# Optimization experiments

Measured on AMD Instinct MI355X. Metric: run time of the kernel, lower is better.

The kernel has to match this reference:

```python
import jax, jax.numpy as jnp
import numpy as np

N, B, H, NH = 16384, 64, 256, 8
MAXN = 512
EPS = 1e-5


def setup_inputs() -> dict:
    key = jax.random.key(0)
    ks = jax.random.split(key, 8)
    s = 0.02
    return {
        "x": jax.random.normal(ks[0], (N, H), jnp.float32),
        "batch": jnp.sort(jax.random.randint(ks[1], (N,), 0, B)),
        "max_nodes": MAXN,
        "norm1_w": jnp.ones((H,), jnp.float32),
        "norm1_b": jnp.zeros((H,), jnp.float32),
        "in_proj_w": jax.random.normal(ks[2], (3 * H, H), jnp.float32) * s,
        "in_proj_b": jnp.zeros((3 * H,), jnp.float32),
        "out_proj_w": jax.random.normal(ks[3], (H, H), jnp.float32) * s,
        "out_proj_b": jnp.zeros((H,), jnp.float32),
        "norm2_w": jnp.ones((H,), jnp.float32),
        "norm2_b": jnp.zeros((H,), jnp.float32),
        "ffn_w1": jax.random.normal(ks[4], (4 * H, H), jnp.float32) * s,
        "ffn_b1": jnp.zeros((4 * H,), jnp.float32),
        "ffn_w2": jax.random.normal(ks[5], (H, 4 * H), jnp.float32) * s,
        "ffn_b2": jnp.zeros((H,), jnp.float32),
    }


def _graph_norm(x, batch, countsf, w, b):
    # Per-graph mean and unbiased std (torch.std default), eps added to std.
    mean = jax.ops.segment_sum(x, batch, num_segments=B) / countsf[:, None]
    c = x - mean[batch]
    var = jax.ops.segment_sum(c * c, batch, num_segments=B) / jnp.maximum(countsf - 1.0, 1.0)[:, None]
    std = jnp.sqrt(var) + EPS
    return w * (c / std[batch]) + b


def _forward(x, batch, max_nodes, norm1_w, norm1_b, in_proj_w, in_proj_b,
             out_proj_w, out_proj_b, norm2_w, norm2_b, ffn_w1, ffn_b1, ffn_w2, ffn_b2):
    n = x.shape[0]
    counts = jax.ops.segment_sum(jnp.ones((n,), jnp.int32), batch, num_segments=B)  # [B]
    countsf = counts.astype(x.dtype)
    starts = jnp.concatenate([jnp.zeros((1,), jnp.int32), jnp.cumsum(counts)[:-1]])
    pos = jnp.arange(n, dtype=jnp.int32) - starts[batch]  # position within graph (batch is sorted)

    # GraphNorm 1, then pack ragged -> padded [B, M, H]
    xn = _graph_norm(x, batch, countsf, norm1_w, norm1_b)
    x_pad = jnp.zeros((B, max_nodes, H), x.dtype).at[batch, pos].set(xn)
    key_valid = jnp.arange(max_nodes)[None, :] < counts[:, None]  # [B, M] True=real node

    # Multi-head attention (eval mode, key_padding_mask)
    qkv = x_pad @ in_proj_w.T + in_proj_b  # [B, M, 3H]
    q, k, v = jnp.split(qkv, 3, axis=-1)
    hd = H // NH
    heads = lambda t: t.reshape(B, max_nodes, NH, hd).transpose(0, 2, 1, 3)  # [B, NH, M, hd]
    q, k, v = heads(q), heads(k), heads(v)
    scores = jnp.einsum('bhqd,bhkd->bhqk', q, k) / np.float32(np.sqrt(hd))
    scores = jnp.where(key_valid[:, None, None, :], scores, jnp.float32(-1e9))
    attn = jax.nn.softmax(scores, axis=-1)
    ctx = jnp.einsum('bhqk,bhkd->bhqd', attn, v).transpose(0, 2, 1, 3).reshape(B, max_nodes, H)
    attn_out = ctx @ out_proj_w.T + out_proj_b

    # Unpack padded -> ragged, residual
    x = x + attn_out[batch, pos]

    # GraphNorm 2 + FFN (exact GELU) + residual
    xn2 = _graph_norm(x, batch, countsf, norm2_w, norm2_b)
    h = jax.nn.gelu(xn2 @ ffn_w1.T + ffn_b1, approximate=False)
    return x + (h @ ffn_w2.T + ffn_b2)


def reference(x, batch, max_nodes, norm1_w, norm1_b, in_proj_w, in_proj_b,
              out_proj_w, out_proj_b, norm2_w, norm2_b, ffn_w1, ffn_b1, ffn_w2, ffn_b2):
    return _forward(x, batch, max_nodes, norm1_w, norm1_b, in_proj_w, in_proj_b,
                    out_proj_w, out_proj_b, norm2_w, norm2_b, ffn_w1, ffn_b1, ffn_w2, ffn_b2)
```

## Files before the change

kernel.cpp:

```cpp
#include <hip/hip_runtime.h>
#include <hip/hip_bf16.h>
#include <math.h>

typedef __bf16 bf16;
typedef bf16 bf16x4 __attribute__((ext_vector_type(4)));
typedef bf16 bf16x8 __attribute__((ext_vector_type(8)));
typedef float f32x4 __attribute__((ext_vector_type(4)));

#define NNODES 16384
#define NB 64
#define HDIM 256
#define NHEADS 8
#define HD 32
#define GN_STRIPS 16

typedef __attribute__((address_space(3))) unsigned int lds_u32;
typedef __attribute__((address_space(1))) const unsigned int glb_u32;

__device__ __forceinline__ void async_copy16(const bf16* gsrc, bf16* ldst) {
    __builtin_amdgcn_global_load_lds((glb_u32*)gsrc, (lds_u32*)ldst, 16, 0, 0);
}

__global__ void cvt_all(const float* __restrict__ pw_q, const float* __restrict__ pw_o,
                        const float* __restrict__ pw_1, const float* __restrict__ pw_2,
                        bf16* __restrict__ dq, bf16* __restrict__ d_o,
                        bf16* __restrict__ d1, bf16* __restrict__ d2,
                        const int* __restrict__ batch, int* __restrict__ starts,
                        int* __restrict__ counts) {
    if (blockIdx.x == 0 && threadIdx.x < 64) {
        int b = threadIdx.x;
        int lo = 0, hi = NNODES;
        while (lo < hi) { int mid = (lo + hi) >> 1; if (batch[mid] < b) lo = mid + 1; else hi = mid; }
        int s0 = lo;
        lo = 0; hi = NNODES;
        while (lo < hi) { int mid = (lo + hi) >> 1; if (batch[mid] < b + 1) lo = mid + 1; else hi = mid; }
        starts[b] = s0;
        counts[b] = lo - s0;
    }
    int i = blockIdx.x * 256 + threadIdx.x;
    const float* src; bf16* dst; int j;
    if (i < 49152)       { src = pw_q; dst = dq;  j = i; }
    else if (i < 65536)  { src = pw_o; dst = d_o; j = i - 49152; }
    else if (i < 131072) { src = pw_1; dst = d1;  j = i - 65536; }
    else                 { src = pw_2; dst = d2;  j = i - 131072; }
    float4 v = *(const float4*)(src + (size_t)j * 4);
    bf16x4 o;
    o[0] = (bf16)v.x; o[1] = (bf16)v.y; o[2] = (bf16)v.z; o[3] = (bf16)v.w;
    *(bf16x4*)(dst + (size_t)j * 4) = o;
}

__global__ __launch_bounds__(256) void gn_partial(
    const float* __restrict__ x, const int* __restrict__ starts,
    const int* __restrict__ counts, float* __restrict__ part) {
    int g = blockIdx.x, strip = blockIdx.y, hh = threadIdx.x;
    int s = starts[g], c = counts[g];
    int chunk = (c + GN_STRIPS - 1) / GN_STRIPS;
    int r0 = strip * chunk, r1 = min(c, r0 + chunk);
    float sum = 0.f, sq = 0.f;
    for (int r = r0; r < r1; ++r) {
        float v = x[(size_t)(s + r) * HDIM + hh];
        sum += v; sq += v * v;
    }
    part[((size_t)(g * GN_STRIPS + strip) * 2 + 0) * HDIM + hh] = sum;
    part[((size_t)(g * GN_STRIPS + strip) * 2 + 1) * HDIM + hh] = sq;
}

__global__ __launch_bounds__(256) void gn_final(
    const float* __restrict__ part, const int* __restrict__ counts,
    const float* __restrict__ w, const float* __restrict__ b, float* __restrict__ stats) {
    int g = blockIdx.x, hh = threadIdx.x;
    float sum = 0.f, sq = 0.f;
    for (int st = 0; st < GN_STRIPS; ++st) {
        sum += part[((size_t)(g * GN_STRIPS + st) * 2 + 0) * HDIM + hh];
        sq  += part[((size_t)(g * GN_STRIPS + st) * 2 + 1) * HDIM + hh];
    }
    float cf = (float)counts[g];
    float mean = sum / cf;
    float var = (sq - cf * mean * mean) / fmaxf(cf - 1.f, 1.f);
    var = fmaxf(var, 0.f);
    float inv = 1.f / (sqrtf(var) + 1e-5f);
    float a = w[hh] * inv;
    stats[(size_t)g * 512 + hh] = a;
    stats[(size_t)g * 512 + 256 + hh] = b[hh] - mean * a;
}

__global__ __launch_bounds__(256) void gn_apply(
    const float* __restrict__ x, const int* __restrict__ batch,
    const float* __restrict__ stats, bf16* __restrict__ out) {
    size_t i = ((size_t)blockIdx.x * 256 + threadIdx.x) * 4;
    int row = (int)(i >> 8);
    int g = batch[row];
    int hh = (int)(i & 255);
    float4 xv = *(const float4*)(x + i);
    float4 av = *(const float4*)(stats + (size_t)g * 512 + hh);
    float4 bv = *(const float4*)(stats + (size_t)g * 512 + 256 + hh);
    bf16x4 o;
    o[0] = (bf16)(av.x * xv.x + bv.x);
    o[1] = (bf16)(av.y * xv.y + bv.y);
    o[2] = (bf16)(av.z * xv.z + bv.z);
    o[3] = (bf16)(av.w * xv.w + bv.w);
    *(bf16x4*)(out + i) = o;
}

template <int MODE>
__global__ __launch_bounds__(256) void gemm_tn(
    const bf16* __restrict__ A, const bf16* __restrict__ B,
    const float* __restrict__ bias, const float* __restrict__ res,
    void* __restrict__ Cout, int M, int N, int K) {
    __shared__ __align__(16) bf16 As[128 * 32];
    __shared__ __align__(16) bf16 Bs[128 * 32];
    const int row0 = blockIdx.x * 128;
    const int col0 = blockIdx.y * 128;
    const int tid = threadIdx.x;
    const int lane = tid & 63;
    const int wave = tid >> 6;
    const int wm = (wave >> 1) * 64;
    const int wn = (wave & 1) * 64;
    const int lr = lane & 15;
    const int lk = lane >> 4;
    const int c0 = tid;
    const int c1 = tid + 256;
    const int r0c = c0 >> 2, o0 = (c0 & 3) * 8;
    const int r1c = c1 >> 2, o1 = (c1 & 3) * 8;

    const bf16* Ab = A + (size_t)row0 * K;
    const bf16* Bb = B + (size_t)col0 * K;

    f32x4 acc[4][4] = {};

    for (int k0 = 0; k0 < K; k0 += 32) {
        __syncthreads();
        async_copy16(Ab + (size_t)r0c * K + k0 + o0, &As[c0 * 8]);
        async_copy16(Ab + (size_t)r1c * K + k0 + o1, &As[c1 * 8]);
        async_copy16(Bb + (size_t)r0c * K + k0 + o0, &Bs[c0 * 8]);
        async_copy16(Bb + (size_t)r1c * K + k0 + o1, &Bs[c1 * 8]);
        __syncthreads();
        bf16x8 af[4], bfr[4];
#pragma unroll
        for (int mi = 0; mi < 4; ++mi)
            af[mi] = *(const bf16x8*)&As[(wm + mi * 16 + lr) * 32 + lk * 8];
#pragma unroll
        for (int ni = 0; ni < 4; ++ni)
            bfr[ni] = *(const bf16x8*)&Bs[(wn + ni * 16 + lr) * 32 + lk * 8];
#pragma unroll
        for (int mi = 0; mi < 4; ++mi)
#pragma unroll
            for (int ni = 0; ni < 4; ++ni)
                acc[mi][ni] = __builtin_amdgcn_mfma_f32_16x16x32_bf16(af[mi], bfr[ni], acc[mi][ni], 0, 0, 0);
    }

#pragma unroll
    for (int mi = 0; mi < 4; ++mi) {
#pragma unroll
        for (int ni = 0; ni < 4; ++ni) {
            const int col = col0 + wn + ni * 16 + lr;
            const float bv = bias[col];
#pragma unroll
            for (int r = 0; r < 4; ++r) {
                const int row = row0 + wm + mi * 16 + lk * 4 + r;
                float v = acc[mi][ni][r] + bv;
                size_t idx = (size_t)row * N + col;
                if (MODE == 0) {
                    ((bf16*)Cout)[idx] = (bf16)v;
                } else if (MODE == 1) {
                    ((float*)Cout)[idx] = v + res[idx];
                } else {
                    float gel = 0.5f * v * (1.f + erff(v * 0.70710678118654752f));
                    ((bf16*)Cout)[idx] = (bf16)gel;
                }
            }
        }
    }
}

__global__ __launch_bounds__(256) void gemm_small_res(
    const bf16* __restrict__ A, const bf16* __restrict__ B,
    const float* __restrict__ bias, const float* __restrict__ res,
    float* __restrict__ Cout, int M, int N, int K) {
    __shared__ __align__(16) bf16 As[64 * 32];
    __shared__ __align__(16) bf16 Bs[64 * 32];
    const int row0 = blockIdx.x * 64;
    const int col0 = blockIdx.y * 64;
    const int tid = threadIdx.x;
    const int lane = tid & 63;
    const int wave = tid >> 6;
    const int wr = (wave >> 1) * 32;
    const int wc = (wave & 1) * 32;
    const int lr = lane & 15;
    const int lk = lane >> 4;
    const int rs = tid >> 2, os = (tid & 3) * 8;

    const bf16* Ab = A + (size_t)row0 * K;
    const bf16* Bb = B + (size_t)col0 * K;

    f32x4 acc[2][2] = {};

    for (int k0 = 0; k0 < K; k0 += 32) {
        __syncthreads();
        async_copy16(Ab + (size_t)rs * K + k0 + os, &As[tid * 8]);
        async_copy16(Bb + (size_t)rs * K + k0 + os, &Bs[tid * 8]);
        __syncthreads();
        bf16x8 af[2], bfr[2];
#pragma unroll
        for (int mi = 0; mi < 2; ++mi)
            af[mi] = *(const bf16x8*)&As[(wr + mi * 16 + lr) * 32 + lk * 8];
#pragma unroll
        for (int ni = 0; ni < 2; ++ni)
            bfr[ni] = *(const bf16x8*)&Bs[(wc + ni * 16 + lr) * 32 + lk * 8];
#pragma unroll
        for (int mi = 0; mi < 2; ++mi)
#pragma unroll
            for (int ni = 0; ni < 2; ++ni)
                acc[mi][ni] = __builtin_amdgcn_mfma_f32_16x16x32_bf16(af[mi], bfr[ni], acc[mi][ni], 0, 0, 0);
    }

#pragma unroll
    for (int mi = 0; mi < 2; ++mi) {
#pragma unroll
        for (int ni = 0; ni < 2; ++ni) {
            const int col = col0 + wc + ni * 16 + lr;
            const float bv = bias[col];
#pragma unroll
            for (int r = 0; r < 4; ++r) {
                const int row = row0 + wr + mi * 16 + lk * 4 + r;
                size_t idx = (size_t)row * N + col;
                Cout[idx] = acc[mi][ni][r] + bv + res[idx];
            }
        }
    }
}

__global__ __launch_bounds__(256) void attn_mfma(
    const bf16* __restrict__ qkv, const int* __restrict__ starts,
    const int* __restrict__ counts, bf16* __restrict__ ctx) {
    int g = blockIdx.x, h = blockIdx.y;
    int s = starts[g], c = counts[g];
    if (c <= 0) return;
    __shared__ __align__(16) bf16 Qs[256][40];
    __shared__ __align__(16) bf16 Ks[64][40];
    __shared__ __align__(16) bf16 Vt[32][72];
    __shared__ __align__(16) bf16 Ps[4][64][72];
    __shared__ float Ls[4][64];
    const int tid = threadIdx.x;
    const int w = tid >> 6, lane = tid & 63;
    const int lo = lane & 15, hi = lane >> 4;
    const float scale = 0.17677669529663687f;
    const int nqc = (c + 255) >> 8;
    const int nkt = (c + 63) >> 6;

    for (int qc = 0; qc < nqc; ++qc) {
        {
            int qrow = qc * 256 + tid;
            const bf16* qp = qkv + (size_t)(s + qrow) * 768 + h * HD;
#pragma unroll
            for (int t4 = 0; t4 < 4; ++t4) {
                bf16x8 sv;
                if (qrow < c) {
                    bf16x8 v = *(const bf16x8*)(qp + t4 * 8);
#pragma unroll
                    for (int u = 0; u < 8; ++u) sv[u] = (bf16)((float)v[u] * scale);
                } else {
#pragma unroll
                    for (int u = 0; u < 8; ++u) sv[u] = (bf16)0.f;
                }
                *(bf16x8*)&Qs[tid][t4 * 8] = sv;
            }
        }
        __syncthreads();
        bf16x8 bq[4];
#pragma unroll
        for (int nt = 0; nt < 4; ++nt) bq[nt] = *(const bf16x8*)&Qs[w * 64 + nt * 16 + lo][hi * 8];

        f32x4 ctxa[4][2] = {};
        float l[4] = {0.f, 0.f, 0.f, 0.f};

        for (int kt = 0; kt < nkt; ++kt) {
            {
                int krow = kt * 64 + (tid >> 2);
                bf16x8 v;
                if (krow < c) v = *(const bf16x8*)(qkv + (size_t)(s + krow) * 768 + 256 + h * HD + (tid & 3) * 8);
                else {
#pragma unroll
                    for (int u = 0; u < 8; ++u) v[u] = (bf16)0.f;
                }
                *(bf16x8*)&Ks[tid >> 2][(tid & 3) * 8] = v;
            }
            {
                int vrow = kt * 64 + (tid & 63);
                int dg = tid >> 6;
                bf16x8 v;
                if (vrow < c) v = *(const bf16x8*)(qkv + (size_t)(s + vrow) * 768 + 512 + h * HD + dg * 8);
                else {
#pragma unroll
                    for (int u = 0; u < 8; ++u) v[u] = (bf16)0.f;
                }
#pragma unroll
                for (int u = 0; u < 8; ++u) Vt[dg * 8 + u][tid & 63] = v[u];
            }
            __syncthreads();

            f32x4 sacc[4][4] = {};
#pragma unroll
            for (int kmt = 0; kmt < 4; ++kmt) {
                bf16x8 ak = *(const bf16x8*)&Ks[kmt * 16 + lo][hi * 8];
#pragma unroll
                for (int nt = 0; nt < 4; ++nt)
                    sacc[kmt][nt] = __builtin_amdgcn_mfma_f32_16x16x32_bf16(ak, bq[nt], sacc[kmt][nt], 0, 0, 0);
            }
#pragma unroll
            for (int kmt = 0; kmt < 4; ++kmt) {
                int kbase = kt * 64 + kmt * 16 + hi * 4;
#pragma unroll
                for (int nt = 0; nt < 4; ++nt) {
                    bf16x4 pv;
#pragma unroll
                    for (int r = 0; r < 4; ++r) {
                        float p = (kbase + r < c) ? __expf(sacc[kmt][nt][r]) : 0.f;
                        l[nt] += p;
                        pv[r] = (bf16)p;
                    }
                    *(bf16x4*)&Ps[w][nt * 16 + lo][kmt * 16 + hi * 4] = pv;
                }
            }
#pragma unroll
            for (int ks = 0; ks < 2; ++ks) {
                bf16x8 bv[2];
#pragma unroll
                for (int dn = 0; dn < 2; ++dn) bv[dn] = *(const bf16x8*)&Vt[dn * 16 + lo][ks * 32 + hi * 8];
#pragma unroll
                for (int qmt = 0; qmt < 4; ++qmt) {
                    bf16x8 ap = *(const bf16x8*)&Ps[w][qmt * 16 + lo][ks * 32 + hi * 8];
#pragma unroll
                    for (int dn = 0; dn < 2; ++dn)
                        ctxa[qmt][dn] = __builtin_amdgcn_mfma_f32_16x16x32_bf16(ap, bv[dn], ctxa[qmt][dn], 0, 0, 0);
                }
            }
            __syncthreads();
        }

#pragma unroll
        for (int nt = 0; nt < 4; ++nt) {
            l[nt] += __shfl_xor(l[nt], 16);
            l[nt] += __shfl_xor(l[nt], 32);
        }
        if (hi == 0) {
#pragma unroll
            for (int nt = 0; nt < 4; ++nt) Ls[w][nt * 16 + lo] = l[nt];
        }
#pragma unroll
        for (int qmt = 0; qmt < 4; ++qmt) {
#pragma unroll
            for (int r = 0; r < 4; ++r) {
                int qrow = qc * 256 + w * 64 + qmt * 16 + hi * 4 + r;
                if (qrow < c) {
                    float linv = 1.f / Ls[w][qmt * 16 + hi * 4 + r];
                    bf16* op = ctx + (size_t)(s + qrow) * HDIM + h * HD;
#pragma unroll
                    for (int dn = 0; dn < 2; ++dn)
                        op[dn * 16 + lo] = (bf16)(ctxa[qmt][dn][r] * linv);
                }
            }
        }
        __syncthreads();
    }
}

extern "C" void kernel_launch(void* const* d_in, const int* in_sizes, int n_in,
                              void* d_out, int out_size, void* d_ws, size_t ws_size,
                              hipStream_t stream) {
    const float* x        = (const float*)d_in[0];
    const int*   batch    = (const int*)d_in[1];
    const float* norm1_w  = (const float*)d_in[3];
    const float* norm1_b  = (const float*)d_in[4];
    const float* in_proj_w  = (const float*)d_in[5];
    const float* in_proj_b  = (const float*)d_in[6];
    const float* out_proj_w = (const float*)d_in[7];
    const float* out_proj_b = (const float*)d_in[8];
    const float* norm2_w  = (const float*)d_in[9];
    const float* norm2_b  = (const float*)d_in[10];
    const float* ffn_w1   = (const float*)d_in[11];
    const float* ffn_b1   = (const float*)d_in[12];
    const float* ffn_w2   = (const float*)d_in[13];
    const float* ffn_b2   = (const float*)d_in[14];
    float* out = (float*)d_out;

    char* ws = (char*)d_ws;
    size_t off = 0;
    auto alloc = [&](size_t bytes) -> void* {
        void* p = ws + off;
        off += bytes;
        off = (off + 255) & ~(size_t)255;
        return p;
    };
    int*  starts = (int*)alloc(NB * 4);
    int*  counts = (int*)alloc(NB * 4);
    bf16* wq = (bf16*)alloc((size_t)768 * 256 * 2);
    bf16* wo = (bf16*)alloc((size_t)256 * 256 * 2);
    bf16* w1 = (bf16*)alloc((size_t)1024 * 256 * 2);
    bf16* w2 = (bf16*)alloc((size_t)256 * 1024 * 2);
    bf16* t0  = (bf16*)alloc((size_t)NNODES * HDIM * 2);
    bf16* qkv = (bf16*)alloc((size_t)NNODES * 768 * 2);
    float* y  = (float*)alloc((size_t)NNODES * HDIM * 4);
    bf16* hbuf = (bf16*)alloc((size_t)NNODES * 1024 * 2);
    float* gnpart = (float*)alloc((size_t)NB * GN_STRIPS * 2 * HDIM * 4);
    float* gnstats = (float*)alloc((size_t)NB * 512 * 4);

    cvt_all<<<196608 / 256, 256, 0, stream>>>(in_proj_w, out_proj_w, ffn_w1, ffn_w2,
                                              wq, wo, w1, w2, batch, starts, counts);
    gn_partial<<<dim3(NB, GN_STRIPS), 256, 0, stream>>>(x, starts, counts, gnpart);
    gn_final<<<NB, 256, 0, stream>>>(gnpart, counts, norm1_w, norm1_b, gnstats);
    gn_apply<<<NNODES * HDIM / 1024, 256, 0, stream>>>(x, batch, gnstats, t0);
    gemm_tn<0><<<dim3(NNODES / 128, 768 / 128), 256, 0, stream>>>(
        t0, wq, in_proj_b, nullptr, qkv, NNODES, 768, 256);
    attn_mfma<<<dim3(NB, NHEADS), 256, 0, stream>>>(qkv, starts, counts, t0);
    gemm_small_res<<<dim3(NNODES / 64, 256 / 64), 256, 0, stream>>>(
        t0, wo, out_proj_b, x, y, NNODES, 256, 256);
    gn_partial<<<dim3(NB, GN_STRIPS), 256, 0, stream>>>(y, starts, counts, gnpart);
    gn_final<<<NB, 256, 0, stream>>>(gnpart, counts, norm2_w, norm2_b, gnstats);
    gn_apply<<<NNODES * HDIM / 1024, 256, 0, stream>>>(y, batch, gnstats, t0);
    gemm_tn<2><<<dim3(NNODES / 128, 1024 / 128), 256, 0, stream>>>(
        t0, w1, ffn_b1, nullptr, hbuf, NNODES, 1024, 256);
    gemm_small_res<<<dim3(NNODES / 64, 256 / 64), 256, 0, stream>>>(
        hbuf, w2, ffn_b2, y, out, NNODES, 256, 1024);
}
```

Before: 237.2 us.

## Double GEMM K-tile with XOR-swizzled LDS and split attention query chunks across blocks

Both GEMM kernels now stage 64-wide K tiles instead of 32, which halves the number of barrier pairs per output tile. They store the tiles in LDS with an XOR swizzle on 16-byte chunks to avoid bank conflicts on the fragment reads. The attention kernel moves its query-chunk loop onto a third grid dimension of size 2, so graphs with more than 256 nodes run on separate blocks and there are more blocks in flight. The cost is double the LDS per GEMM block, which may reduce occupancy, and extra blocks that exit immediately for small graphs.

```diff
diff --git a/kernel.cpp b/kernel.cpp
--- a/kernel.cpp
+++ b/kernel.cpp
@@ -107,8 +107,8 @@
     const bf16* __restrict__ A, const bf16* __restrict__ B,
     const float* __restrict__ bias, const float* __restrict__ res,
     void* __restrict__ Cout, int M, int N, int K) {
-    __shared__ __align__(16) bf16 As[128 * 32];
-    __shared__ __align__(16) bf16 Bs[128 * 32];
+    __shared__ __align__(16) bf16 As[128 * 64];
+    __shared__ __align__(16) bf16 Bs[128 * 64];
     const int row0 = blockIdx.x * 128;
     const int col0 = blockIdx.y * 128;
     const int tid = threadIdx.x;
@@ -118,35 +118,49 @@
     const int wn = (wave & 1) * 64;
     const int lr = lane & 15;
     const int lk = lane >> 4;
-    const int c0 = tid;
-    const int c1 = tid + 256;
-    const int r0c = c0 >> 2, o0 = (c0 & 3) * 8;
-    const int r1c = c1 >> 2, o1 = (c1 & 3) * 8;
 
     const bf16* Ab = A + (size_t)row0 * K;
     const bf16* Bb = B + (size_t)col0 * K;
 
+    int srow[4], soff[4];
+#pragma unroll
+    for (int q = 0; q < 4; ++q) {
+        int c = tid + q * 256;
+        int r = c >> 3;
+        srow[q] = r;
+        soff[q] = ((c & 7) ^ (r & 7)) * 8;
+    }
+
     f32x4 acc[4][4] = {};
 
-    for (int k0 = 0; k0 < K; k0 += 32) {
-        __syncthreads();
-        async_copy16(Ab + (size_t)r0c * K + k0 + o0, &As[c0 * 8]);
-        async_copy16(Ab + (size_t)r1c * K + k0 + o1, &As[c1 * 8]);
-        async_copy16(Bb + (size_t)r0c * K + k0 + o0, &Bs[c0 * 8]);
-        async_copy16(Bb + (size_t)r1c * K + k0 + o1, &Bs[c1 * 8]);
-        __syncthreads();
-        bf16x8 af[4], bfr[4];
-#pragma unroll
-        for (int mi = 0; mi < 4; ++mi)
-            af[mi] = *(const bf16x8*)&As[(wm + mi * 16 + lr) * 32 + lk * 8];
-#pragma unroll
-        for (int ni = 0; ni < 4; ++ni)
-            bfr[ni] = *(const bf16x8*)&Bs[(wn + ni * 16 + lr) * 32 + lk * 8];
-#pragma unroll
-        for (int mi = 0; mi < 4; ++mi)
-#pragma unroll
-            for (int ni = 0; ni < 4; ++ni)
-                acc[mi][ni] = __builtin_amdgcn_mfma_f32_16x16x32_bf16(af[mi], bfr[ni], acc[mi][ni], 0, 0, 0);
+    for (int k0 = 0; k0 < K; k0 += 64) {
+        __syncthreads();
+#pragma unroll
+        for (int q = 0; q < 4; ++q)
+            async_copy16(Ab + (size_t)srow[q] * K + k0 + soff[q], &As[(tid + q * 256) * 8]);
+#pragma unroll
+        for (int q = 0; q < 4; ++q)
+            async_copy16(Bb + (size_t)srow[q] * K + k0 + soff[q], &Bs[(tid + q * 256) * 8]);
+        __syncthreads();
+#pragma unroll
+        for (int ks = 0; ks < 2; ++ks) {
+            bf16x8 af[4], bfr[4];
+#pragma unroll
+            for (int mi = 0; mi < 4; ++mi) {
+                int r = wm + mi * 16 + lr;
+                af[mi] = *(const bf16x8*)&As[r * 64 + ((ks * 4 + lk) ^ (r & 7)) * 8];
+            }
+#pragma unroll
+            for (int ni = 0; ni < 4; ++ni) {
+                int r = wn + ni * 16 + lr;
+                bfr[ni] = *(const bf16x8*)&Bs[r * 64 + ((ks * 4 + lk) ^ (r & 7)) * 8];
+            }
+#pragma unroll
+            for (int mi = 0; mi < 4; ++mi)
+#pragma unroll
+                for (int ni = 0; ni < 4; ++ni)
+                    acc[mi][ni] = __builtin_amdgcn_mfma_f32_16x16x32_bf16(af[mi], bfr[ni], acc[mi][ni], 0, 0, 0);
+        }
     }
 
 #pragma unroll
@@ -177,8 +191,8 @@
     const bf16* __restrict__ A, const bf16* __restrict__ B,
     const float* __restrict__ bias, const float* __restrict__ res,
     float* __restrict__ Cout, int M, int N, int K) {
-    __shared__ __align__(16) bf16 As[64 * 32];
-    __shared__ __align__(16) bf16 Bs[64 * 32];
+    __shared__ __align__(16) bf16 As[64 * 64];
+    __shared__ __align__(16) bf16 Bs[64 * 64];
     const int row0 = blockIdx.x * 64;
     const int col0 = blockIdx.y * 64;
     const int tid = threadIdx.x;
@@ -188,30 +202,49 @@
     const int wc = (wave & 1) * 32;
     const int lr = lane & 15;
     const int lk = lane >> 4;
-    const int rs = tid >> 2, os = (tid & 3) * 8;
 
     const bf16* Ab = A + (size_t)row0 * K;
     const bf16* Bb = B + (size_t)col0 * K;
 
+    int srow[2], soff[2];
+#pragma unroll
+    for (int q = 0; q < 2; ++q) {
+        int c = tid + q * 256;
+        int r = c >> 3;
+        srow[q] = r;
+        soff[q] = ((c & 7) ^ (r & 7)) * 8;
+    }
+
     f32x4 acc[2][2] = {};
 
-    for (int k0 = 0; k0 < K; k0 += 32) {
-        __syncthreads();
-        async_copy16(Ab + (size_t)rs * K + k0 + os, &As[tid * 8]);
-        async_copy16(Bb + (size_t)rs * K + k0 + os, &Bs[tid * 8]);
-        __syncthreads();
-        bf16x8 af[2], bfr[2];
-#pragma unroll
-        for (int mi = 0; mi < 2; ++mi)
-            af[mi] = *(const bf16x8*)&As[(wr + mi * 16 + lr) * 32 + lk * 8];
-#pragma unroll
-        for (int ni = 0; ni < 2; ++ni)
-            bfr[ni] = *(const bf16x8*)&Bs[(wc + ni * 16 + lr) * 32 + lk * 8];
-#pragma unroll
-        for (int mi = 0; mi < 2; ++mi)
-#pragma unroll
-            for (int ni = 0; ni < 2; ++ni)
-                acc[mi][ni] = __builtin_amdgcn_mfma_f32_16x16x32_bf16(af[mi], bfr[ni], acc[mi][ni], 0, 0, 0);
+    for (int k0 = 0; k0 < K; k0 += 64) {
+        __syncthreads();
+#pragma unroll
+        for (int q = 0; q < 2; ++q)
+            async_copy16(Ab + (size_t)srow[q] * K + k0 + soff[q], &As[(tid + q * 256) * 8]);
+#pragma unroll
+        for (int q = 0; q < 2; ++q)
+            async_copy16(Bb + (size_t)srow[q] * K + k0 + soff[q], &Bs[(tid + q * 256) * 8]);
+        __syncthreads();
+#pragma unroll
+        for (int ks = 0; ks < 2; ++ks) {
+            bf16x8 af[2], bfr[2];
+#pragma unroll
+            for (int mi = 0; mi < 2; ++mi) {
+                int r = wr + mi * 16 + lr;
+                af[mi] = *(const bf16x8*)&As[r * 64 + ((ks * 4 + lk) ^ (r & 7)) * 8];
+            }
+#pragma unroll
+            for (int ni = 0; ni < 2; ++ni) {
+                int r = wc + ni * 16 + lr;
+                bfr[ni] = *(const bf16x8*)&Bs[r * 64 + ((ks * 4 + lk) ^ (r & 7)) * 8];
+            }
+#pragma unroll
+            for (int mi = 0; mi < 2; ++mi)
+#pragma unroll
+                for (int ni = 0; ni < 2; ++ni)
+                    acc[mi][ni] = __builtin_amdgcn_mfma_f32_16x16x32_bf16(af[mi], bfr[ni], acc[mi][ni], 0, 0, 0);
+        }
     }
 
 #pragma unroll
@@ -233,9 +266,9 @@
 __global__ __launch_bounds__(256) void attn_mfma(
     const bf16* __restrict__ qkv, const int* __restrict__ starts,
     const int* __restrict__ counts, bf16* __restrict__ ctx) {
-    int g = blockIdx.x, h = blockIdx.y;
+    int g = blockIdx.x, h = blockIdx.y, qc = blockIdx.z;
     int s = starts[g], c = counts[g];
-    if (c <= 0) return;
+    if (qc * 256 >= c) return;
     __shared__ __align__(16) bf16 Qs[256][40];
     __shared__ __align__(16) bf16 Ks[64][40];
     __shared__ __align__(16) bf16 Vt[32][72];
@@ -245,123 +278,119 @@
     const int w = tid >> 6, lane = tid & 63;
     const int lo = lane & 15, hi = lane >> 4;
     const float scale = 0.17677669529663687f;
-    const int nqc = (c + 255) >> 8;
     const int nkt = (c + 63) >> 6;
 
-    for (int qc = 0; qc < nqc; ++qc) {
+    {
+        int qrow = qc * 256 + tid;
+        const bf16* qp = qkv + (size_t)(s + qrow) * 768 + h * HD;
+#pragma unroll
+        for (int t4 = 0; t4 < 4; ++t4) {
+            bf16x8 sv;
+            if (qrow < c) {
+                bf16x8 v = *(const bf16x8*)(qp + t4 * 8);
+#pragma unroll
+                for (int u = 0; u < 8; ++u) sv[u] = (bf16)((float)v[u] * scale);
+            } else {
+#pragma unroll
+                for (int u = 0; u < 8; ++u) sv[u] = (bf16)0.f;
+            }
+            *(bf16x8*)&Qs[tid][t4 * 8] = sv;
+        }
+    }
+    __syncthreads();
+    bf16x8 bq[4];
+#pragma unroll
+    for (int nt = 0; nt < 4; ++nt) bq[nt] = *(const bf16x8*)&Qs[w * 64 + nt * 16 + lo][hi * 8];
+
+    f32x4 ctxa[4][2] = {};
+    float l[4] = {0.f, 0.f, 0.f, 0.f};
+
+    for (int kt = 0; kt < nkt; ++kt) {
         {
-            int qrow = qc * 256 + tid;
-            const bf16* qp = qkv + (size_t)(s + qrow) * 768 + h * HD;
-#pragma unroll
-            for (int t4 = 0; t4 < 4; ++t4) {
-                bf16x8 sv;
-                if (qrow < c) {
-                    bf16x8 v = *(const bf16x8*)(qp + t4 * 8);
-#pragma unroll
-                    for (int u = 0; u < 8; ++u) sv[u] = (bf16)((float)v[u] * scale);
-                } else {
-#pragma unroll
-                    for (int u = 0; u < 8; ++u) sv[u] = (bf16)0.f;
+            int krow = kt * 64 + (tid >> 2);
+            bf16x8 v;
+            if (krow < c) v = *(const bf16x8*)(qkv + (size_t)(s + krow) * 768 + 256 + h * HD + (tid & 3) * 8);
+            else {
+#pragma unroll
+                for (int u = 0; u < 8; ++u) v[u] = (bf16)0.f;
+            }
+            *(bf16x8*)&Ks[tid >> 2][(tid & 3) * 8] = v;
+        }
+        {
+            int vrow = kt * 64 + (tid & 63);
+            int dg = tid >> 6;
+            bf16x8 v;
+            if (vrow < c) v = *(const bf16x8*)(qkv + (size_t)(s + vrow) * 768 + 512 + h * HD + dg * 8);
+            else {
+#pragma unroll
+                for (int u = 0; u < 8; ++u) v[u] = (bf16)0.f;
+            }
+#pragma unroll
+            for (int u = 0; u < 8; ++u) Vt[dg * 8 + u][tid & 63] = v[u];
+        }
+        __syncthreads();
+
+        f32x4 sacc[4][4] = {};
+#pragma unroll
+        for (int kmt = 0; kmt < 4; ++kmt) {
+            bf16x8 ak = *(const bf16x8*)&Ks[kmt * 16 + lo][hi * 8];
+#pragma unroll
+            for (int nt = 0; nt < 4; ++nt)
+                sacc[kmt][nt] = __builtin_amdgcn_mfma_f32_16x16x32_bf16(ak, bq[nt], sacc[kmt][nt], 0, 0, 0);
+        }
+#pragma unroll
+        for (int kmt = 0; kmt < 4; ++kmt) {
+            int kbase = kt * 64 + kmt * 16 + hi * 4;
+#pragma unroll
+            for (int nt = 0; nt < 4; ++nt) {
+                bf16x4 pv;
+#pragma unroll
+                for (int r = 0; r < 4; ++r) {
+                    float p = (kbase + r < c) ? __expf(sacc[kmt][nt][r]) : 0.f;
+                    l[nt] += p;
+                    pv[r] = (bf16)p;
                 }
-                *(bf16x8*)&Qs[tid][t4 * 8] = sv;
-            }
-        }
-        __syncthreads();
-        bf16x8 bq[4];
-#pragma unroll
-        for (int nt = 0; nt < 4; ++nt) bq[nt] = *(const bf16x8*)&Qs[w * 64 + nt * 16 + lo][hi * 8];
-
-        f32x4 ctxa[4][2] = {};
-        float l[4] = {0.f, 0.f, 0.f, 0.f};
-
-        for (int kt = 0; kt < nkt; ++kt) {
-            {
-                int krow = kt * 64 + (tid >> 2);
-                bf16x8 v;
-                if (krow < c) v = *(const bf16x8*)(qkv + (size_t)(s + krow) * 768 + 256 + h * HD + (tid & 3) * 8);
-                else {
-#pragma unroll
-                    for (int u = 0; u < 8; ++u) v[u] = (bf16)0.f;
-                }
-                *(bf16x8*)&Ks[tid >> 2][(tid & 3) * 8] = v;
-            }
-            {
-                int vrow = kt * 64 + (tid & 63);
-                int dg = tid >> 6;
-                bf16x8 v;
-                if (vrow < c) v = *(const bf16x8*)(qkv + (size_t)(s + vrow) * 768 + 512 + h * HD + dg * 8);
-                else {
-#pragma unroll
-                    for (int u = 0; u < 8; ++u) v[u] = (bf16)0.f;
-                }
-#pragma unroll
-                for (int u = 0; u < 8; ++u) Vt[dg * 8 + u][tid & 63] = v[u];
-            }
-            __syncthreads();
-
-            f32x4 sacc[4][4] = {};
-#pragma unroll
-            for (int kmt = 0; kmt < 4; ++kmt) {
-                bf16x8 ak = *(const bf16x8*)&Ks[kmt * 16 + lo][hi * 8];
-#pragma unroll
-                for (int nt = 0; nt < 4; ++nt)
-                    sacc[kmt][nt] = __builtin_amdgcn_mfma_f32_16x16x32_bf16(ak, bq[nt], sacc[kmt][nt], 0, 0, 0);
-            }
-#pragma unroll
-            for (int kmt = 0; kmt < 4; ++kmt) {
-                int kbase = kt * 64 + kmt * 16 + hi * 4;
-#pragma unroll
-                for (int nt = 0; nt < 4; ++nt) {
-                    bf16x4 pv;
-#pragma unroll
-                    for (int r = 0; r < 4; ++r) {
-                        float p = (kbase + r < c) ? __expf(sacc[kmt][nt][r]) : 0.f;
-                        l[nt] += p;
-                        pv[r] = (bf16)p;
-                    }
-                    *(bf16x4*)&Ps[w][nt * 16 + lo][kmt * 16 + hi * 4] = pv;
-                }
-            }
-#pragma unroll
-            for (int ks = 0; ks < 2; ++ks) {
-                bf16x8 bv[2];
-#pragma unroll
-                for (int dn = 0; dn < 2; ++dn) bv[dn] = *(const bf16x8*)&Vt[dn * 16 + lo][ks * 32 + hi * 8];
-#pragma unroll
-                for (int qmt = 0; qmt < 4; ++qmt) {
-                    bf16x8 ap = *(const bf16x8*)&Ps[w][qmt * 16 + lo][ks * 32 + hi * 8];
-#pragma unroll
-                    for (int dn = 0; dn < 2; ++dn)
-                        ctxa[qmt][dn] = __builtin_amdgcn_mfma_f32_16x16x32_bf16(ap, bv[dn], ctxa[qmt][dn], 0, 0, 0);
-                }
-            }
-            __syncthreads();
-        }
-
-#pragma unroll
-        for (int nt = 0; nt < 4; ++nt) {
-            l[nt] += __shfl_xor(l[nt], 16);
-            l[nt] += __shfl_xor(l[nt], 32);
-        }
-        if (hi == 0) {
-#pragma unroll
-            for (int nt = 0; nt < 4; ++nt) Ls[w][nt * 16 + lo] = l[nt];
-        }
-#pragma unroll
-        for (int qmt = 0; qmt < 4; ++qmt) {
-#pragma unroll
-            for (int r = 0; r < 4; ++r) {
-                int qrow = qc * 256 + w * 64 + qmt * 16 + hi * 4 + r;
-                if (qrow < c) {
-                    float linv = 1.f / Ls[w][qmt * 16 + hi * 4 + r];
-                    bf16* op = ctx + (size_t)(s + qrow) * HDIM + h * HD;
-#pragma unroll
-                    for (int dn = 0; dn < 2; ++dn)
-                        op[dn * 16 + lo] = (bf16)(ctxa[qmt][dn][r] * linv);
-                }
-            }
-        }
-        __syncthreads();
+                *(bf16x4*)&Ps[w][nt * 16 + lo][kmt * 16 + hi * 4] = pv;
+            }
+        }
+#pragma unroll
+        for (int ks = 0; ks < 2; ++ks) {
+            bf16x8 bv[2];
+#pragma unroll
+            for (int dn = 0; dn < 2; ++dn) bv[dn] = *(const bf16x8*)&Vt[dn * 16 + lo][ks * 32 + hi * 8];
+#pragma unroll
+            for (int qmt = 0; qmt < 4; ++qmt) {
+                bf16x8 ap = *(const bf16x8*)&Ps[w][qmt * 16 + lo][ks * 32 + hi * 8];
+#pragma unroll
+                for (int dn = 0; dn < 2; ++dn)
+                    ctxa[qmt][dn] = __builtin_amdgcn_mfma_f32_16x16x32_bf16(ap, bv[dn], ctxa[qmt][dn], 0, 0, 0);
+            }
+        }
+        __syncthreads();
+    }
+
+#pragma unroll
+    for (int nt = 0; nt < 4; ++nt) {
+        l[nt] += __shfl_xor(l[nt], 16);
+        l[nt] += __shfl_xor(l[nt], 32);
+    }
+    if (hi == 0) {
+#pragma unroll
+        for (int nt = 0; nt < 4; ++nt) Ls[w][nt * 16 + lo] = l[nt];
+    }
+#pragma unroll
+    for (int qmt = 0; qmt < 4; ++qmt) {
+#pragma unroll
+        for (int r = 0; r < 4; ++r) {
+            int qrow = qc * 256 + w * 64 + qmt * 16 + hi * 4 + r;
+            if (qrow < c) {
+                float linv = 1.f / Ls[w][qmt * 16 + hi * 4 + r];
+                bf16* op = ctx + (size_t)(s + qrow) * HDIM + h * HD;
+#pragma unroll
+                for (int dn = 0; dn < 2; ++dn)
+                    op[dn * 16 + lo] = (bf16)(ctxa[qmt][dn][r] * linv);
+            }
+        }
     }
 }
 
@@ -412,7 +441,7 @@
     gn_apply<<<NNODES * HDIM / 1024, 256, 0, stream>>>(x, batch, gnstats, t0);
     gemm_tn<0><<<dim3(NNODES / 128, 768 / 128), 256, 0, stream>>>(
         t0, wq, in_proj_b, nullptr, qkv, NNODES, 768, 256);
-    attn_mfma<<<dim3(NB, NHEADS), 256, 0, stream>>>(qkv, starts, counts, t0);
+    attn_mfma<<<dim3(NB, NHEADS, 2), 256, 0, stream>>>(qkv, starts, counts, t0);
     gemm_small_res<<<dim3(NNODES / 64, 256 / 64), 256, 0, stream>>>(
         t0, wo, out_proj_b, x, y, NNODES, 256, 256);
     gn_partial<<<dim3(NB, GN_STRIPS), 256, 0, stream>>>(y, starts, counts, gnpart);
```

After: 224.0 us. 1.06x faster.

## Double-buffer GEMM LDS tiles and split attention query chunks across grid

Applied to the files above, without the earlier changes.

Both GEMM kernels now use two LDS buffers and issue async copies for the next K tile before computing on the current one. This removes one barrier per iteration and overlaps loads with MFMA work. The attention kernel moves its serial loop over 256-row query chunks into a third grid dimension of size 2, so graphs with more than 256 nodes are processed by two blocks in parallel. The cost is double the GEMM LDS footprint, which may lower occupancy, and K/V tiles that are re-read by each chunk block.

```diff
diff --git a/kernel.cpp b/kernel.cpp
--- a/kernel.cpp
+++ b/kernel.cpp
@@ -107,8 +107,8 @@
     const bf16* __restrict__ A, const bf16* __restrict__ B,
     const float* __restrict__ bias, const float* __restrict__ res,
     void* __restrict__ Cout, int M, int N, int K) {
-    __shared__ __align__(16) bf16 As[128 * 32];
-    __shared__ __align__(16) bf16 Bs[128 * 32];
+    __shared__ __align__(16) bf16 As[2][128 * 32];
+    __shared__ __align__(16) bf16 Bs[2][128 * 32];
     const int row0 = blockIdx.x * 128;
     const int col0 = blockIdx.y * 128;
     const int tid = threadIdx.x;
@@ -128,25 +128,32 @@
 
     f32x4 acc[4][4] = {};
 
-    for (int k0 = 0; k0 < K; k0 += 32) {
-        __syncthreads();
-        async_copy16(Ab + (size_t)r0c * K + k0 + o0, &As[c0 * 8]);
-        async_copy16(Ab + (size_t)r1c * K + k0 + o1, &As[c1 * 8]);
-        async_copy16(Bb + (size_t)r0c * K + k0 + o0, &Bs[c0 * 8]);
-        async_copy16(Bb + (size_t)r1c * K + k0 + o1, &Bs[c1 * 8]);
-        __syncthreads();
+    auto stage = [&](int buf, int k0) {
+        async_copy16(Ab + (size_t)r0c * K + k0 + o0, &As[buf][c0 * 8]);
+        async_copy16(Ab + (size_t)r1c * K + k0 + o1, &As[buf][c1 * 8]);
+        async_copy16(Bb + (size_t)r0c * K + k0 + o0, &Bs[buf][c0 * 8]);
+        async_copy16(Bb + (size_t)r1c * K + k0 + o1, &Bs[buf][c1 * 8]);
+    };
+
+    const int nk = K >> 5;
+    stage(0, 0);
+    __syncthreads();
+    for (int t = 0; t < nk; ++t) {
+        const int cur = t & 1;
+        if (t + 1 < nk) stage(cur ^ 1, (t + 1) << 5);
         bf16x8 af[4], bfr[4];
 #pragma unroll
         for (int mi = 0; mi < 4; ++mi)
-            af[mi] = *(const bf16x8*)&As[(wm + mi * 16 + lr) * 32 + lk * 8];
+            af[mi] = *(const bf16x8*)&As[cur][(wm + mi * 16 + lr) * 32 + lk * 8];
 #pragma unroll
         for (int ni = 0; ni < 4; ++ni)
-            bfr[ni] = *(const bf16x8*)&Bs[(wn + ni * 16 + lr) * 32 + lk * 8];
+            bfr[ni] = *(const bf16x8*)&Bs[cur][(wn + ni * 16 + lr) * 32 + lk * 8];
 #pragma unroll
         for (int mi = 0; mi < 4; ++mi)
 #pragma unroll
             for (int ni = 0; ni < 4; ++ni)
                 acc[mi][ni] = __builtin_amdgcn_mfma_f32_16x16x32_bf16(af[mi], bfr[ni], acc[mi][ni], 0, 0, 0);
+        __syncthreads();
     }
 
 #pragma unroll
@@ -177,8 +184,8 @@
     const bf16* __restrict__ A, const bf16* __restrict__ B,
     const float* __restrict__ bias, const float* __restrict__ res,
     float* __restrict__ Cout, int M, int N, int K) {
-    __shared__ __align__(16) bf16 As[64 * 32];
-    __shared__ __align__(16) bf16 Bs[64 * 32];
+    __shared__ __align__(16) bf16 As[2][64 * 32];
+    __shared__ __align__(16) bf16 Bs[2][64 * 32];
     const int row0 = blockIdx.x * 64;
     const int col0 = blockIdx.y * 64;
     const int tid = threadIdx.x;
@@ -195,23 +202,30 @@
 
     f32x4 acc[2][2] = {};
 
-    for (int k0 = 0; k0 < K; k0 += 32) {
-        __syncthreads();
-        async_copy16(Ab + (size_t)rs * K + k0 + os, &As[tid * 8]);
-        async_copy16(Bb + (size_t)rs * K + k0 + os, &Bs[tid * 8]);
-        __syncthreads();
+    auto stage = [&](int buf, int k0) {
+        async_copy16(Ab + (size_t)rs * K + k0 + os, &As[buf][tid * 8]);
+        async_copy16(Bb + (size_t)rs * K + k0 + os, &Bs[buf][tid * 8]);
+    };
+
+    const int nk = K >> 5;
+    stage(0, 0);
+    __syncthreads();
+    for (int t = 0; t < nk; ++t) {
+        const int cur = t & 1;
+        if (t + 1 < nk) stage(cur ^ 1, (t + 1) << 5);
         bf16x8 af[2], bfr[2];
 #pragma unroll
         for (int mi = 0; mi < 2; ++mi)
-            af[mi] = *(const bf16x8*)&As[(wr + mi * 16 + lr) * 32 + lk * 8];
+            af[mi] = *(const bf16x8*)&As[cur][(wr + mi * 16 + lr) * 32 + lk * 8];
 #pragma unroll
         for (int ni = 0; ni < 2; ++ni)
-            bfr[ni] = *(const bf16x8*)&Bs[(wc + ni * 16 + lr) * 32 + lk * 8];
+            bfr[ni] = *(const bf16x8*)&Bs[cur][(wc + ni * 16 + lr) * 32 + lk * 8];
 #pragma unroll
         for (int mi = 0; mi < 2; ++mi)
 #pragma unroll
             for (int ni = 0; ni < 2; ++ni)
                 acc[mi][ni] = __builtin_amdgcn_mfma_f32_16x16x32_bf16(af[mi], bfr[ni], acc[mi][ni], 0, 0, 0);
+        __syncthreads();
     }
 
 #pragma unroll
@@ -233,9 +247,9 @@
 __global__ __launch_bounds__(256) void attn_mfma(
     const bf16* __restrict__ qkv, const int* __restrict__ starts,
     const int* __restrict__ counts, bf16* __restrict__ ctx) {
-    int g = blockIdx.x, h = blockIdx.y;
+    int g = blockIdx.x, h = blockIdx.y, qc = blockIdx.z;
     int s = starts[g], c = counts[g];
-    if (c <= 0) return;
+    if (qc * 256 >= c) return;
     __shared__ __align__(16) bf16 Qs[256][40];
     __shared__ __align__(16) bf16 Ks[64][40];
     __shared__ __align__(16) bf16 Vt[32][72];
@@ -245,123 +259,119 @@
     const int w = tid >> 6, lane = tid & 63;
     const int lo = lane & 15, hi = lane >> 4;
     const float scale = 0.17677669529663687f;
-    const int nqc = (c + 255) >> 8;
     const int nkt = (c + 63) >> 6;
 
-    for (int qc = 0; qc < nqc; ++qc) {
+    {
+        int qrow = qc * 256 + tid;
+        const bf16* qp = qkv + (size_t)(s + qrow) * 768 + h * HD;
+#pragma unroll
+        for (int t4 = 0; t4 < 4; ++t4) {
+            bf16x8 sv;
+            if (qrow < c) {
+                bf16x8 v = *(const bf16x8*)(qp + t4 * 8);
+#pragma unroll
+                for (int u = 0; u < 8; ++u) sv[u] = (bf16)((float)v[u] * scale);
+            } else {
+#pragma unroll
+                for (int u = 0; u < 8; ++u) sv[u] = (bf16)0.f;
+            }
+            *(bf16x8*)&Qs[tid][t4 * 8] = sv;
+        }
+    }
+    __syncthreads();
+    bf16x8 bq[4];
+#pragma unroll
+    for (int nt = 0; nt < 4; ++nt) bq[nt] = *(const bf16x8*)&Qs[w * 64 + nt * 16 + lo][hi * 8];
+
+    f32x4 ctxa[4][2] = {};
+    float l[4] = {0.f, 0.f, 0.f, 0.f};
+
+    for (int kt = 0; kt < nkt; ++kt) {
         {
-            int qrow = qc * 256 + tid;
-            const bf16* qp = qkv + (size_t)(s + qrow) * 768 + h * HD;
-#pragma unroll
-            for (int t4 = 0; t4 < 4; ++t4) {
-                bf16x8 sv;
-                if (qrow < c) {
-                    bf16x8 v = *(const bf16x8*)(qp + t4 * 8);
-#pragma unroll
-                    for (int u = 0; u < 8; ++u) sv[u] = (bf16)((float)v[u] * scale);
-                } else {
-#pragma unroll
-                    for (int u = 0; u < 8; ++u) sv[u] = (bf16)0.f;
+            int krow = kt * 64 + (tid >> 2);
+            bf16x8 v;
+            if (krow < c) v = *(const bf16x8*)(qkv + (size_t)(s + krow) * 768 + 256 + h * HD + (tid & 3) * 8);
+            else {
+#pragma unroll
+                for (int u = 0; u < 8; ++u) v[u] = (bf16)0.f;
+            }
+            *(bf16x8*)&Ks[tid >> 2][(tid & 3) * 8] = v;
+        }
+        {
+            int vrow = kt * 64 + (tid & 63);
+            int dg = tid >> 6;
+            bf16x8 v;
+            if (vrow < c) v = *(const bf16x8*)(qkv + (size_t)(s + vrow) * 768 + 512 + h * HD + dg * 8);
+            else {
+#pragma unroll
+                for (int u = 0; u < 8; ++u) v[u] = (bf16)0.f;
+            }
+#pragma unroll
+            for (int u = 0; u < 8; ++u) Vt[dg * 8 + u][tid & 63] = v[u];
+        }
+        __syncthreads();
+
+        f32x4 sacc[4][4] = {};
+#pragma unroll
+        for (int kmt = 0; kmt < 4; ++kmt) {
+            bf16x8 ak = *(const bf16x8*)&Ks[kmt * 16 + lo][hi * 8];
+#pragma unroll
+            for (int nt = 0; nt < 4; ++nt)
+                sacc[kmt][nt] = __builtin_amdgcn_mfma_f32_16x16x32_bf16(ak, bq[nt], sacc[kmt][nt], 0, 0, 0);
+        }
+#pragma unroll
+        for (int kmt = 0; kmt < 4; ++kmt) {
+            int kbase = kt * 64 + kmt * 16 + hi * 4;
+#pragma unroll
+            for (int nt = 0; nt < 4; ++nt) {
+                bf16x4 pv;
+#pragma unroll
+                for (int r = 0; r < 4; ++r) {
+                    float p = (kbase + r < c) ? __expf(sacc[kmt][nt][r]) : 0.f;
+                    l[nt] += p;
+                    pv[r] = (bf16)p;
                 }
-                *(bf16x8*)&Qs[tid][t4 * 8] = sv;
+                *(bf16x4*)&Ps[w][nt * 16 + lo][kmt * 16 + hi * 4] = pv;
+            }
+        }
+#pragma unroll
+        for (int ks = 0; ks < 2; ++ks) {
+            bf16x8 bv[2];
+#pragma unroll
+            for (int dn = 0; dn < 2; ++dn) bv[dn] = *(const bf16x8*)&Vt[dn * 16 + lo][ks * 32 + hi * 8];
+#pragma unroll
+            for (int qmt = 0; qmt < 4; ++qmt) {
+                bf16x8 ap = *(const bf16x8*)&Ps[w][qmt * 16 + lo][ks * 32 + hi * 8];
+#pragma unroll
+                for (int dn = 0; dn < 2; ++dn)
+                    ctxa[qmt][dn] = __builtin_amdgcn_mfma_f32_16x16x32_bf16(ap, bv[dn], ctxa[qmt][dn], 0, 0, 0);
             }
         }
         __syncthreads();
-        bf16x8 bq[4];
-#pragma unroll
-        for (int nt = 0; nt < 4; ++nt) bq[nt] = *(const bf16x8*)&Qs[w * 64 + nt * 16 + lo][hi * 8];
-
-        f32x4 ctxa[4][2] = {};
-        float l[4] = {0.f, 0.f, 0.f, 0.f};
-
-        for (int kt = 0; kt < nkt; ++kt) {
-            {
-                int krow = kt * 64 + (tid >> 2);
-                bf16x8 v;
-                if (krow < c) v = *(const bf16x8*)(qkv + (size_t)(s + krow) * 768 + 256 + h * HD + (tid & 3) * 8);
-                else {
-#pragma unroll
-                    for (int u = 0; u < 8; ++u) v[u] = (bf16)0.f;
-                }
-                *(bf16x8*)&Ks[tid >> 2][(tid & 3) * 8] = v;
-            }
-            {
-                int vrow = kt * 64 + (tid & 63);
-                int dg = tid >> 6;
-                bf16x8 v;
-                if (vrow < c) v = *(const bf16x8*)(qkv + (size_t)(s + vrow) * 768 + 512 + h * HD + dg * 8);
-                else {
-#pragma unroll
-                    for (int u = 0; u < 8; ++u) v[u] = (bf16)0.f;
-                }
-#pragma unroll
-                for (int u = 0; u < 8; ++u) Vt[dg * 8 + u][tid & 63] = v[u];
-            }
-            __syncthreads();
-
-            f32x4 sacc[4][4] = {};
-#pragma unroll
-            for (int kmt = 0; kmt < 4; ++kmt) {
-                bf16x8 ak = *(const bf16x8*)&Ks[kmt * 16 + lo][hi * 8];
-#pragma unroll
-                for (int nt = 0; nt < 4; ++nt)
-                    sacc[kmt][nt] = __builtin_amdgcn_mfma_f32_16x16x32_bf16(ak, bq[nt], sacc[kmt][nt], 0, 0, 0);
-            }
-#pragma unroll
-            for (int kmt = 0; kmt < 4; ++kmt) {
-                int kbase = kt * 64 + kmt * 16 + hi * 4;
-#pragma unroll
-                for (int nt = 0; nt < 4; ++nt) {
-                    bf16x4 pv;
-#pragma unroll
-                    for (int r = 0; r < 4; ++r) {
-                        float p = (kbase + r < c) ? __expf(sacc[kmt][nt][r]) : 0.f;
-                        l[nt] += p;
-                        pv[r] = (bf16)p;
-                    }
-                    *(bf16x4*)&Ps[w][nt * 16 + lo][kmt * 16 + hi * 4] = pv;
-                }
-            }
-#pragma unroll
-            for (int ks = 0; ks < 2; ++ks) {
-                bf16x8 bv[2];
-#pragma unroll
-                for (int dn = 0; dn < 2; ++dn) bv[dn] = *(const bf16x8*)&Vt[dn * 16 + lo][ks * 32 + hi * 8];
-#pragma unroll
-                for (int qmt = 0; qmt < 4; ++qmt) {
-                    bf16x8 ap = *(const bf16x8*)&Ps[w][qmt * 16 + lo][ks * 32 + hi * 8];
-#pragma unroll
-                    for (int dn = 0; dn < 2; ++dn)
-                        ctxa[qmt][dn] = __builtin_amdgcn_mfma_f32_16x16x32_bf16(ap, bv[dn], ctxa[qmt][dn], 0, 0, 0);
-                }
-            }
-            __syncthreads();
-        }
-
-#pragma unroll
-        for (int nt = 0; nt < 4; ++nt) {
-            l[nt] += __shfl_xor(l[nt], 16);
-            l[nt] += __shfl_xor(l[nt], 32);
-        }
-        if (hi == 0) {
-#pragma unroll
-            for (int nt = 0; nt < 4; ++nt) Ls[w][nt * 16 + lo] = l[nt];
-        }
-#pragma unroll
-        for (int qmt = 0; qmt < 4; ++qmt) {
-#pragma unroll
-            for (int r = 0; r < 4; ++r) {
-                int qrow = qc * 256 + w * 64 + qmt * 16 + hi * 4 + r;
-                if (qrow < c) {
-                    float linv = 1.f / Ls[w][qmt * 16 + hi * 4 + r];
-                    bf16* op = ctx + (size_t)(s + qrow) * HDIM + h * HD;
-#pragma unroll
-                    for (int dn = 0; dn < 2; ++dn)
-                        op[dn * 16 + lo] = (bf16)(ctxa[qmt][dn][r] * linv);
-                }
-            }
-        }
-        __syncthreads();
+    }
+
+#pragma unroll
+    for (int nt = 0; nt < 4; ++nt) {
+        l[nt] += __shfl_xor(l[nt], 16);
+        l[nt] += __shfl_xor(l[nt], 32);
+    }
+    if (hi == 0) {
+#pragma unroll
+        for (int nt = 0; nt < 4; ++nt) Ls[w][nt * 16 + lo] = l[nt];
+    }
+#pragma unroll
+    for (int qmt = 0; qmt < 4; ++qmt) {
+#pragma unroll
+        for (int r = 0; r < 4; ++r) {
+            int qrow = qc * 256 + w * 64 + qmt * 16 + hi * 4 + r;
+            if (qrow < c) {
+                float linv = 1.f / Ls[w][qmt * 16 + hi * 4 + r];
+                bf16* op = ctx + (size_t)(s + qrow) * HDIM + h * HD;
+#pragma unroll
+                for (int dn = 0; dn < 2; ++dn)
+                    op[dn * 16 + lo] = (bf16)(ctxa[qmt][dn][r] * linv);
+            }
+        }
     }
 }
 
@@ -412,7 +422,7 @@
     gn_apply<<<NNODES * HDIM / 1024, 256, 0, stream>>>(x, batch, gnstats, t0);
     gemm_tn<0><<<dim3(NNODES / 128, 768 / 128), 256, 0, stream>>>(
         t0, wq, in_proj_b, nullptr, qkv, NNODES, 768, 256);
-    attn_mfma<<<dim3(NB, NHEADS), 256, 0, stream>>>(qkv, starts, counts, t0);
+    attn_mfma<<<dim3(NB, NHEADS, 2), 256, 0, stream>>>(qkv, starts, counts, t0);
     gemm_small_res<<<dim3(NNODES / 64, 256 / 64), 256, 0, stream>>>(
         t0, wo, out_proj_b, x, y, NNODES, 256, 256);
     gn_partial<<<dim3(NB, GN_STRIPS), 256, 0, stream>>>(y, starts, counts, gnpart);
```

New measurement: 233.6 us. No clear change (-1.5%).
